# Kernel optimization log

Measured on AMD Instinct MI355X. Metric: run time of the kernel, lower is better.

The kernel has to match this reference:

```python
import jax, jax.numpy as jnp
import numpy as np

N_NODES = 10000
N_EDGES = 640000
IN_CH = 128
HID = 128
OUT = 2


def setup_inputs() -> dict:
    key = jax.random.key(0)
    ks = jax.random.split(key, 12)
    s_in = 1.0 / np.sqrt(IN_CH)
    s_2h = 1.0 / np.sqrt(2 * HID)
    s_h = 1.0 / np.sqrt(HID)
    return {
        "x": jax.random.normal(ks[0], (N_NODES, IN_CH), dtype=jnp.float32),
        "edge_index": jax.random.randint(ks[1], (2, N_EDGES), 0, N_NODES, dtype=jnp.int64),
        # SAGEConv: lin_l applied to aggregated neighbors (has bias), lin_r to self (no bias)
        "W_l": jax.random.uniform(ks[2], (IN_CH, HID), jnp.float32, -s_in, s_in),
        "b_l": jax.random.uniform(ks[3], (HID,), jnp.float32, -s_in, s_in),
        "W_r": jax.random.uniform(ks[4], (IN_CH, HID), jnp.float32, -s_in, s_in),
        # lin0: in -> hid
        "W0": jax.random.uniform(ks[5], (IN_CH, HID), jnp.float32, -s_in, s_in),
        "b0": jax.random.uniform(ks[6], (HID,), jnp.float32, -s_in, s_in),
        # lin1: 2*hid -> hid
        "W1": jax.random.uniform(ks[7], (2 * HID, HID), jnp.float32, -s_2h, s_2h),
        "b1": jax.random.uniform(ks[8], (HID,), jnp.float32, -s_2h, s_2h),
        # lin2: hid -> out
        "W2": jax.random.uniform(ks[9], (HID, OUT), jnp.float32, -s_h, s_h),
        "b2": jax.random.uniform(ks[10], (OUT,), jnp.float32, -s_h, s_h),
    }


def reference(x, edge_index, W_l, b_l, W_r, W0, b0, W1, b1, W2, b2):
    src, dst = edge_index[0], edge_index[1]
    # SAGE mean aggregation: gather source features, scatter-mean onto dst nodes
    msgs = x[src]                                                # [E, in]
    agg = jax.ops.segment_sum(msgs, dst, num_segments=N_NODES)  # [N, in]
    deg = jax.ops.segment_sum(jnp.ones((src.shape[0],), x.dtype), dst,
                              num_segments=N_NODES)              # [N]
    agg = agg / jnp.maximum(deg, 1.0)[:, None]
    # SAGEConv output: lin_l(agg) + lin_r(x)
    h = agg @ W_l + b_l + x @ W_r                                # [N, hid]
    h = jax.nn.relu(h)
    h = jnp.max(h, axis=-2)                                      # [hid] global max pool over nodes
    # concat branch: news node is x[0]
    news = jax.nn.relu(x[0] @ W0 + b0)                           # [hid]
    h = jax.nn.relu(jnp.concatenate([news, h], axis=-1) @ W1 + b1)
    return h @ W2 + b2                                           # [out]
```

## Files before the change

### kernel.cpp

```cpp
#include <hip/hip_runtime.h>
#include <hip/hip_bf16.h>

#define NCH 128
#define NPART 256
#define NRANGE 512
#define SEGCAP 24
#define RCAP 2560
#define PSMAX 32

typedef __attribute__((ext_vector_type(8))) short bfrag;
typedef __attribute__((ext_vector_type(4))) float ffrag;
typedef __attribute__((ext_vector_type(2))) float f32x2;

__device__ inline unsigned int f2bf_pair(float lo, float hi) {
    unsigned int ul = __float_as_uint(lo);
    unsigned int uh = __float_as_uint(hi);
    ul = (ul + 0x7fffu + ((ul >> 16) & 1u)) >> 16;
    uh = (uh + 0x7fffu + ((uh >> 16) & 1u)) & 0xffff0000u;
    return (ul & 0xffffu) | uh;
}

__global__ __launch_bounds__(256) void k_partprep(
    const float2* __restrict__ x2, const float* __restrict__ Wl,
    const float* __restrict__ Wr, const int* __restrict__ ei32,
    const long long* __restrict__ ei64, unsigned int* __restrict__ M32,
    unsigned int* __restrict__ Wt32, unsigned short* __restrict__ xq,
    unsigned int* __restrict__ seg, int* __restrict__ segcnt,
    unsigned int* __restrict__ hmaxU, int* __restrict__ done,
    int n2, int N, int E, int PSr) {
    const int t = threadIdx.x;
    if (blockIdx.x < NPART) {
        if (blockIdx.x == 0) {
            if (t < 128) hmaxU[t] = 0u;
            if (t == 128) *done = 0;
        }
        __shared__ int sflag;
        __shared__ int cur[NRANGE];
        if (t < 64) {
            int v = ei32[2 * t + 1];
            unsigned long long b = __ballot(v != 0);
            if (t == 0) sflag = (b == 0ULL) ? 1 : 0;
        }
        for (int i = t; i < NRANGE; i += 256) cur[i] = 0;
        __syncthreads();
        const int flag = sflag;
        const int b = blockIdx.x;
        const int ES = (E + NPART - 1) / NPART;
        const int e0 = b * ES, e1 = min(E, e0 + ES);
        for (int bb = e0; bb < e1; bb += 1024) {
            int ebase = bb + t * 4;
            int m = min(4, e1 - ebase);
            if (m <= 0) continue;
            int src4[4], dst4[4];
            if (flag) {
#pragma unroll
                for (int j = 0; j < 4; ++j) {
                    if (j < m) {
                        src4[j] = (int)ei64[ebase + j];
                        dst4[j] = (int)ei64[(size_t)E + ebase + j];
                    }
                }
            } else {
#pragma unroll
                for (int j = 0; j < 4; ++j) {
                    if (j < m) {
                        src4[j] = ei32[ebase + j];
                        dst4[j] = ei32[(size_t)E + ebase + j];
                    }
                }
            }
#pragma unroll
            for (int j = 0; j < 4; ++j) {
                if (j < m) {
                    int r = dst4[j] / PSr;
                    int dl = dst4[j] - r * PSr;
                    int pos = atomicAdd(&cur[r], 1);
                    if (pos < SEGCAP)
                        seg[((size_t)b * NRANGE + r) * SEGCAP + pos] =
                            ((unsigned int)dl << 16) | (unsigned int)src4[j];
                }
            }
        }
        __syncthreads();
        for (int i = t; i < NRANGE; i += 256)
            segcnt[b * NRANGE + i] = min(cur[i], SEGCAP);
        return;
    }
    int i = (int)(blockIdx.x - NPART) * 256 + t;
    if (i < n2) {
        float2 v = x2[i];
        int n = i >> 6, c = i & 63;
        M32[n * 128 + 64 + c] = f2bf_pair(v.x, v.y);
        xq[i] = (unsigned short)__builtin_amdgcn_cvt_pk_fp8_f32(v.x, v.y, 0u, false);
        return;
    }
    int j = i - n2;
    if (j < 128 * 128) {
        int c = j & 127, kp = j >> 7;
        int k0 = 2 * kp, k1 = 2 * kp + 1;
        float v0 = (k0 < 128) ? Wl[k0 * 128 + c] : Wr[(k0 - 128) * 128 + c];
        float v1 = (k1 < 128) ? Wl[k1 * 128 + c] : Wr[(k1 - 128) * 128 + c];
        Wt32[c * 128 + kp] = f2bf_pair(v0, v1);
    }
}

__global__ __launch_bounds__(512) void k_aggdense(
    const unsigned int* __restrict__ seg, const int* __restrict__ segcnt,
    const unsigned int* __restrict__ M32, const unsigned short* __restrict__ xq,
    const short* __restrict__ Wt, const float* __restrict__ bl,
    unsigned int* __restrict__ hmaxU, int* __restrict__ done,
    const float* __restrict__ x,
    const float* __restrict__ W0, const float* __restrict__ b0,
    const float* __restrict__ W1, const float* __restrict__ b1,
    const float* __restrict__ W2, const float* __restrict__ b2,
    float* __restrict__ out, int N, int PSr) {
    __shared__ unsigned int tmp[RCAP];
    __shared__ unsigned short scsr[RCAP];
    __shared__ unsigned int aggL[PSMAX * 66];
    __shared__ int sc[NPART];
    __shared__ int hist[PSMAX], startp[PSMAX], cur[PSMAX];
    __shared__ float red[8][32];
    __shared__ int lastflag;
    const int r = blockIdx.x;
    const int t = threadIdx.x;

    int mycnt = 0;
    if (t < NPART) { mycnt = segcnt[t * NRANGE + r]; sc[t] = mycnt; }
    for (int i = t; i < PSMAX * 66; i += 512) aggL[i] = 0;
    if (t < PSMAX) hist[t] = 0;
    __syncthreads();
    for (int off = 1; off < NPART; off <<= 1) {
        int v = (t >= off && t < NPART) ? sc[t - off] : 0;
        __syncthreads();
        if (t < NPART) sc[t] += v;
        __syncthreads();
    }
    const int total = min(sc[NPART - 1], RCAP);

    if (t < NPART && mycnt > 0) {
        int excl = sc[t] - mycnt;
        const uint4* sp = (const uint4*)(seg + ((size_t)t * NRANGE + r) * SEGCAP);
        for (int k = 0; k < mycnt; k += 4) {
            uint4 v = sp[k >> 2];
            unsigned int w[4] = {v.x, v.y, v.z, v.w};
#pragma unroll
            for (int j = 0; j < 4; ++j) {
                if (k + j < mycnt) {
                    unsigned int e = w[j];
                    tmp[excl + k + j] = e;
                    atomicAdd(&hist[e >> 16], 1);
                }
            }
        }
    }
    __syncthreads();
    if (t == 0) {
        int run = 0;
#pragma unroll
        for (int i = 0; i < PSMAX; ++i) { startp[i] = run; cur[i] = run; run += hist[i]; }
    }
    __syncthreads();
    for (int i = t; i < total; i += 512) {
        unsigned int v = tmp[i];
        int pos = atomicAdd(&cur[v >> 16], 1);
        scsr[pos] = (unsigned short)(v & 0xffffu);
    }
    __syncthreads();

    const int wave = t >> 6, lane = t & 63;
    for (int li = wave; li < PSr; li += 8) {
        int node = r * PSr + li;
        if (node >= N) break;
        int base = startp[li], d = hist[li];
        float ax = 0.f, ay = 0.f;
        int i = 0;
        for (; i + 16 <= d; i += 16) {
            int s[16];
            unsigned short u[16];
#pragma unroll
            for (int j = 0; j < 16; ++j) s[j] = scsr[base + i + j];
#pragma unroll
            for (int j = 0; j < 16; ++j) u[j] = xq[s[j] * 64 + lane];
#pragma unroll
            for (int j = 0; j < 16; ++j) {
                f32x2 v = __builtin_amdgcn_cvt_pk_f32_fp8((unsigned int)u[j], false);
                ax += v.x; ay += v.y;
            }
        }
        for (; i + 8 <= d; i += 8) {
            int s[8];
            unsigned short u[8];
#pragma unroll
            for (int j = 0; j < 8; ++j) s[j] = scsr[base + i + j];
#pragma unroll
            for (int j = 0; j < 8; ++j) u[j] = xq[s[j] * 64 + lane];
#pragma unroll
            for (int j = 0; j < 8; ++j) {
                f32x2 v = __builtin_amdgcn_cvt_pk_f32_fp8((unsigned int)u[j], false);
                ax += v.x; ay += v.y;
            }
        }
        for (; i < d; ++i) {
            unsigned short u = xq[((int)scsr[base + i]) * 64 + lane];
            f32x2 v = __builtin_amdgcn_cvt_pk_f32_fp8((unsigned int)u, false);
            ax += v.x; ay += v.y;
        }
        float sca = 1.0f / fmaxf((float)d, 1.0f);
        aggL[li * 66 + lane] = f2bf_pair(ax * sca, ay * sca);
    }
    __syncthreads();

    const int l16 = lane & 15, quad = lane >> 4;
    const int rt = wave & 1, cg = wave >> 1;
    const int lrow = rt * 16 + l16;
    bfrag a[8];
#pragma unroll
    for (int kk = 0; kk < 4; ++kk)
        a[kk] = *(const bfrag*)((const short*)(aggL + lrow * 66 + kk * 16 + quad * 4));
    {
        int mc = min(r * PSr + lrow, N - 1);
#pragma unroll
        for (int kk = 0; kk < 4; ++kk)
            a[4 + kk] = *(const bfrag*)((const short*)(M32 + (size_t)mc * 128 + 64)
                                        + kk * 32 + quad * 8);
    }
    float mx[2];
#pragma unroll
    for (int ct = 0; ct < 2; ++ct) {
        int col = cg * 32 + ct * 16 + l16;
        float bv = bl[col];
        ffrag acc = {bv, bv, bv, bv};
        const short* wp = Wt + (size_t)col * 256 + quad * 8;
#pragma unroll
        for (int kk = 0; kk < 8; ++kk) {
            bfrag b = *(const bfrag*)(wp + kk * 32);
            acc = __builtin_amdgcn_mfma_f32_16x16x32_bf16(a[kk], b, acc, 0, 0, 0);
        }
        float lm = 0.f;
#pragma unroll
        for (int rr = 0; rr < 4; ++rr) {
            int lr = rt * 16 + quad * 4 + rr;
            int nd = r * PSr + lr;
            if (lr < PSr && nd < N) lm = fmaxf(lm, fmaxf(acc[rr], 0.f));
        }
        lm = fmaxf(lm, __shfl_xor(lm, 16));
        lm = fmaxf(lm, __shfl_xor(lm, 32));
        mx[ct] = lm;
    }
    if (lane < 16) {
        red[wave][l16]      = mx[0];
        red[wave][16 + l16] = mx[1];
    }
    __syncthreads();
    if (t < 128) {
        int cg2 = t >> 5, wi = t & 31;
        float v = fmaxf(red[2 * cg2][wi], red[2 * cg2 + 1][wi]);
        atomicMax(&hmaxU[t], __float_as_uint(v));
    }

    __syncthreads();
    if (t == 0) {
        __threadfence();
        int old = atomicAdd(done, 1);
        lastflag = (old == NRANGE - 1) ? 1 : 0;
    }
    __syncthreads();
    if (!lastflag) return;
    __threadfence();

    float* hs   = (float*)tmp;
    float* cat  = hs;
    float* part = hs + 256;
    float* h1p  = hs + 768;
    float* pr   = hs + 896;
    float* xsp  = hs + 1152;
    const int c = t & 127, sg = t >> 7;
    if (t < 128) {
        xsp[t] = x[t];
        cat[128 + t] = __uint_as_float(atomicOr(&hmaxU[t], 0u));
    }
    __syncthreads();
    {
        float a0 = 0.f, a1 = 0.f, a2 = 0.f, a3 = 0.f;
        int k0 = sg * 32;
#pragma unroll
        for (int j = 0; j < 32; j += 4) {
            a0 += xsp[k0 + j + 0] * W0[(k0 + j + 0) * NCH + c];
            a1 += xsp[k0 + j + 1] * W0[(k0 + j + 1) * NCH + c];
            a2 += xsp[k0 + j + 2] * W0[(k0 + j + 2) * NCH + c];
            a3 += xsp[k0 + j + 3] * W0[(k0 + j + 3) * NCH + c];
        }
        part[sg * 128 + c] = (a0 + a1) + (a2 + a3);
    }
    __syncthreads();
    if (t < 128)
        cat[t] = fmaxf(b0[t] + part[t] + part[128 + t] + part[256 + t] + part[384 + t], 0.f);
    __syncthreads();
    {
        float a0 = 0.f, a1 = 0.f, a2 = 0.f, a3 = 0.f;
        int k0 = sg * 64;
#pragma unroll
        for (int j = 0; j < 64; j += 4) {
            a0 += cat[k0 + j + 0] * W1[(k0 + j + 0) * NCH + c];
            a1 += cat[k0 + j + 1] * W1[(k0 + j + 1) * NCH + c];
            a2 += cat[k0 + j + 2] * W1[(k0 + j + 2) * NCH + c];
            a3 += cat[k0 + j + 3] * W1[(k0 + j + 3) * NCH + c];
        }
        part[sg * 128 + c] = (a0 + a1) + (a2 + a3);
    }
    __syncthreads();
    if (t < 128)
        h1p[t] = fmaxf(b1[t] + part[t] + part[128 + t] + part[256 + t] + part[384 + t], 0.f);
    __syncthreads();
    if (t < 128) {
        float2 w = ((const float2*)W2)[t];
        pr[t]       = h1p[t] * w.x;
        pr[128 + t] = h1p[t] * w.y;
    }
    __syncthreads();
    for (int off = 64; off >= 1; off >>= 1) {
        if (t < off) { pr[t] += pr[t + off]; pr[128 + t] += pr[128 + t + off]; }
        __syncthreads();
    }
    if (t == 0) out[0] = pr[0] + b2[0];
    if (t == 1) out[1] = pr[128] + b2[1];
}

__global__ void k_detect(const int* __restrict__ ei, int* __restrict__ flag) {
    int v = ei[2 * threadIdx.x + 1];
    unsigned long long b = __ballot(v != 0);
    if (threadIdx.x == 0) *flag = (b == 0ULL) ? 1 : 0;
}
__global__ void k_hist(const int* __restrict__ ei32, const long long* __restrict__ ei64,
                       const int* __restrict__ flag, int* __restrict__ cnt, int E) {
    int e = blockIdx.x * blockDim.x + threadIdx.x;
    if (e >= E) return;
    int dst = (*flag) ? (int)ei64[(size_t)E + e] : ei32[(size_t)E + e];
    atomicAdd(&cnt[dst], 1);
}
__global__ void k_scan(const int* __restrict__ cnt, int* __restrict__ row_start, int N) {
    __shared__ int lds[1024];
    int t = threadIdx.x;
    int chunk = (N + 1023) / 1024;
    int base = t * chunk;
    int sum = 0;
    for (int i = 0; i < chunk; ++i) {
        int idx = base + i;
        if (idx < N) sum += cnt[idx];
    }
    lds[t] = sum;
    __syncthreads();
    for (int off = 1; off < 1024; off <<= 1) {
        int v = (t >= off) ? lds[t - off] : 0;
        __syncthreads();
        lds[t] += v;
        __syncthreads();
    }
    int run = (t == 0) ? 0 : lds[t - 1];
    for (int i = 0; i < chunk; ++i) {
        int idx = base + i;
        if (idx < N) { row_start[idx] = run; run += cnt[idx]; }
    }
    if (t == 1023) row_start[N] = run;
}
__global__ void k_fill(const int* __restrict__ ei32, const long long* __restrict__ ei64,
                       const int* __restrict__ flag, const int* __restrict__ row_start,
                       int* __restrict__ cursor, int* __restrict__ csr, int E) {
    int e = blockIdx.x * blockDim.x + threadIdx.x;
    if (e >= E) return;
    int src, dst;
    if (*flag) { src = (int)ei64[e]; dst = (int)ei64[(size_t)E + e]; }
    else       { src = ei32[e];      dst = ei32[(size_t)E + e]; }
    int pos = atomicAdd(&cursor[dst], 1);
    csr[row_start[dst] + pos] = src;
}
__global__ __launch_bounds__(256) void k_agg_linmax(
    const float* __restrict__ x, const int* __restrict__ row_start,
    const int* __restrict__ csr, const float* __restrict__ Wl,
    const float* __restrict__ bl, const float* __restrict__ Wr,
    unsigned int* __restrict__ hmaxU, int N, int E) {
    const int lane = threadIdx.x & 63;
    const int wave = threadIdx.x >> 6;
    const int group = blockIdx.x * 4 + wave;
    const int ngroups = (N + 3) / 4;
    const float2* __restrict__ x2  = (const float2*)x;
    const float2* __restrict__ Wl2 = (const float2*)Wl;
    const float2* __restrict__ Wr2 = (const float2*)Wr;
    const float2* __restrict__ bl2 = (const float2*)bl;
    float2 m = make_float2(0.f, 0.f);
    if (group < ngroups) {
        int n0 = group * 4;
        int s[4], d[4];
#pragma unroll
        for (int q = 0; q < 4; ++q) {
            int n = n0 + q;
            if (n < N) { s[q] = row_start[n]; d[q] = row_start[n + 1] - s[q]; }
            else       { s[q] = 0; d[q] = 0; }
        }
        int maxd = max(max(d[0], d[1]), max(d[2], d[3]));
        float2 acc[4];
#pragma unroll
        for (int q = 0; q < 4; ++q) acc[q] = make_float2(0.f, 0.f);
        int idxv[4] = {0, 0, 0, 0};
        for (int i = 0; i < maxd; ++i) {
            int t = i & 63;
            if (t == 0) {
#pragma unroll
                for (int q = 0; q < 4; ++q) {
                    if (i < d[q]) {
                        int a = s[q] + i + lane;
                        a = (a < E) ? a : (E - 1);
                        idxv[q] = csr[a];
                    }
                }
            }
#pragma unroll
            for (int q = 0; q < 4; ++q) {
                if (i < d[q]) {
                    int src = __shfl(idxv[q], t);
                    float2 v = x2[src * 64 + lane];
                    acc[q].x += v.x; acc[q].y += v.y;
                }
            }
        }
        float2 xv[4];
#pragma unroll
        for (int q = 0; q < 4; ++q) {
            float sc = 1.0f / fmaxf((float)d[q], 1.0f);
            acc[q].x *= sc; acc[q].y *= sc;
            int n = n0 + q;
            xv[q] = (n < N) ? x2[n * 64 + lane] : make_float2(0.f, 0.f);
        }
        float2 o[4];
#pragma unroll
        for (int q = 0; q < 4; ++q) o[q] = bl2[lane];
        for (int j = 0; j < 64; ++j) {
            float2 wl0 = Wl2[(2 * j) * 64 + lane];
            float2 wl1 = Wl2[(2 * j + 1) * 64 + lane];
            float2 wr0 = Wr2[(2 * j) * 64 + lane];
            float2 wr1 = Wr2[(2 * j + 1) * 64 + lane];
#pragma unroll
            for (int q = 0; q < 4; ++q) {
                float ax = __shfl(acc[q].x, j);
                float ay = __shfl(acc[q].y, j);
                float xx = __shfl(xv[q].x, j);
                float xy = __shfl(xv[q].y, j);
                o[q].x += ax * wl0.x + ay * wl1.x + xx * wr0.x + xy * wr1.x;
                o[q].y += ax * wl0.y + ay * wl1.y + xx * wr0.y + xy * wr1.y;
            }
        }
#pragma unroll
        for (int q = 0; q < 4; ++q) {
            if (n0 + q < N) {
                m.x = fmaxf(m.x, fmaxf(o[q].x, 0.f));
                m.y = fmaxf(m.y, fmaxf(o[q].y, 0.f));
            }
        }
    }
    __shared__ float2 red2[4][64];
    red2[wave][lane] = m;
    __syncthreads();
    if (wave == 0) {
#pragma unroll
        for (int ww = 1; ww < 4; ++ww) {
            m.x = fmaxf(m.x, red2[ww][lane].x);
            m.y = fmaxf(m.y, red2[ww][lane].y);
        }
        atomicMax(&hmaxU[2 * lane],     __float_as_uint(m.x));
        atomicMax(&hmaxU[2 * lane + 1], __float_as_uint(m.y));
    }
}
__global__ void k_head_fb(const float* __restrict__ x, const float* __restrict__ hmax,
                          const float* __restrict__ W0, const float* __restrict__ b0,
                          const float* __restrict__ W1, const float* __restrict__ b1,
                          const float* __restrict__ W2, const float* __restrict__ b2,
                          float* __restrict__ out) {
    __shared__ float s_cat[2 * NCH];
    __shared__ float s_part[256];
    __shared__ float s_h1[NCH];
    int t = threadIdx.x;
    if (t < NCH) {
        float acc = b0[t];
        for (int k = 0; k < NCH; ++k) acc += x[k] * W0[k * NCH + t];
        s_cat[t] = fmaxf(acc, 0.f);
        s_cat[NCH + t] = hmax[t];
    }
    __syncthreads();
    {
        int c = t & 127, half = t >> 7;
        float p = 0.f;
        int k0 = half * NCH;
        for (int k = k0; k < k0 + NCH; ++k) p += s_cat[k] * W1[k * NCH + c];
        s_part[t] = p;
    }
    __syncthreads();
    if (t < NCH) s_h1[t] = fmaxf(s_part[t] + s_part[NCH + t] + b1[t], 0.f);
    __syncthreads();
    if (t < 2) {
        float o = b2[t];
        for (int k = 0; k < NCH; ++k) o += s_h1[k] * W2[k * 2 + t];
        out[t] = o;
    }
}

extern "C" void kernel_launch(void* const* d_in, const int* in_sizes, int n_in,
                              void* d_out, int out_size, void* d_ws, size_t ws_size,
                              hipStream_t stream) {
    const float* x  = (const float*)d_in[0];
    const void*  ei = d_in[1];
    const float* Wl = (const float*)d_in[2];
    const float* bl = (const float*)d_in[3];
    const float* Wr = (const float*)d_in[4];
    const float* W0 = (const float*)d_in[5];
    const float* b0 = (const float*)d_in[6];
    const float* W1 = (const float*)d_in[7];
    const float* b1 = (const float*)d_in[8];
    const float* W2 = (const float*)d_in[9];
    const float* b2 = (const float*)d_in[10];
    float* out = (float*)d_out;

    const int N = in_sizes[0] / NCH;
    const int E = in_sizes[1] / 2;
    const int n2 = N * 64;
    const int PSr = (N + NRANGE - 1) / NRANGE;

    int* iws = (int*)d_ws;
    unsigned int* hmaxU = (unsigned int*)iws;
    int* done = iws + 128;
    int* segcnt = iws + 192;
    unsigned int* seg = (unsigned int*)(segcnt + NPART * NRANGE);
    unsigned int* Wt32 = seg + (size_t)NPART * NRANGE * SEGCAP;
    unsigned int* M32  = Wt32 + 128 * 128;
    unsigned short* xq = (unsigned short*)(M32 + (size_t)N * 128);
    size_t need = ((size_t)192 + NPART * NRANGE +
                   (size_t)NPART * NRANGE * SEGCAP + 128 * 128 +
                   (size_t)N * 128 + (size_t)N * 32) * 4;
    bool main_ok = (need <= ws_size) && (N <= NRANGE * PSMAX) && (N <= 65535) &&
                   (PSr >= 1) && (PSr <= PSMAX);

    if (main_ok) {
        int prepb = (n2 + 128 * 128 + 255) / 256;
        k_partprep<<<NPART + prepb, 256, 0, stream>>>(
            (const float2*)x, Wl, Wr, (const int*)ei, (const long long*)ei,
            M32, Wt32, xq, seg, segcnt, hmaxU, done, n2, N, E, PSr);
        k_aggdense<<<NRANGE, 512, 0, stream>>>(seg, segcnt, M32, xq,
                                               (const short*)Wt32,
                                               bl, hmaxU, done, x,
                                               W0, b0, W1, b1, W2, b2, out, N, PSr);
        return;
    }

    int* fcnt      = iws;
    int* fcursor   = iws + N;
    unsigned int* fhmax = (unsigned int*)(iws + 2 * N);
    int* flag      = iws + 2 * N + 128;
    int* frs       = iws + 2 * N + 132;
    int* fcsr      = iws + 3 * N + 144;

    hipMemsetAsync(d_ws, 0, (size_t)(2 * N + 128) * sizeof(int), stream);
    k_detect<<<1, 64, 0, stream>>>((const int*)ei, flag);
    k_hist<<<(E + 255) / 256, 256, 0, stream>>>((const int*)ei, (const long long*)ei,
                                                flag, fcnt, E);
    k_scan<<<1, 1024, 0, stream>>>(fcnt, frs, N);
    k_fill<<<(E + 255) / 256, 256, 0, stream>>>((const int*)ei, (const long long*)ei,
                                                flag, frs, fcursor, fcsr, E);
    int ngroups = (N + 3) / 4;
    k_agg_linmax<<<(ngroups + 3) / 4, 256, 0, stream>>>(x, frs, fcsr, Wl, bl, Wr,
                                                        fhmax, N, E);
    k_head_fb<<<1, 256, 0, stream>>>(x, (const float*)fhmax, W0, b0, W1, b1, W2, b2, out);
}
```

Before: 122.8 us.

## Widen fp8 gather to 4 channels per lane, use wave-shuffle scans and magic division

The neighbor gather now has each half-wave load 32-bit words holding four fp8 channels and process alternate edges, then combines the halves with a cross-half shuffle. This aims for fewer, wider gather loads and more memory parallelism per wave. The block-wide prefix sums over partitions and histogram bins become wave shuffle scans to cut barriers, and the per-edge division by PSr becomes a precomputed multiply-high. The prep kernel also vectorizes the x conversion to float4. The tail path now gathers with clamped indices, which may do redundant loads.

```diff
diff --git a/kernel.cpp b/kernel.cpp
--- a/kernel.cpp
+++ b/kernel.cpp
@@ -21,13 +21,13 @@
 }
 
 __global__ __launch_bounds__(256) void k_partprep(
-    const float2* __restrict__ x2, const float* __restrict__ Wl,
+    const float4* __restrict__ x4, const float* __restrict__ Wl,
     const float* __restrict__ Wr, const int* __restrict__ ei32,
     const long long* __restrict__ ei64, unsigned int* __restrict__ M32,
-    unsigned int* __restrict__ Wt32, unsigned short* __restrict__ xq,
+    unsigned int* __restrict__ Wt32, unsigned int* __restrict__ xqU,
     unsigned int* __restrict__ seg, int* __restrict__ segcnt,
     unsigned int* __restrict__ hmaxU, int* __restrict__ done,
-    int n2, int N, int E, int PSr) {
+    int nq, int N, int E, int PSr, unsigned int Mdiv) {
     const int t = threadIdx.x;
     if (blockIdx.x < NPART) {
         if (blockIdx.x == 0) {
@@ -72,8 +72,9 @@
 #pragma unroll
             for (int j = 0; j < 4; ++j) {
                 if (j < m) {
-                    int r = dst4[j] / PSr;
-                    int dl = dst4[j] - r * PSr;
+                    int dstj = dst4[j];
+                    int r = Mdiv ? (int)__umulhi((unsigned int)dstj, Mdiv) : dstj;
+                    int dl = dstj - r * PSr;
                     int pos = atomicAdd(&cur[r], 1);
                     if (pos < SEGCAP)
                         seg[((size_t)b * NRANGE + r) * SEGCAP + pos] =
@@ -87,14 +88,18 @@
         return;
     }
     int i = (int)(blockIdx.x - NPART) * 256 + t;
-    if (i < n2) {
-        float2 v = x2[i];
-        int n = i >> 6, c = i & 63;
-        M32[n * 128 + 64 + c] = f2bf_pair(v.x, v.y);
-        xq[i] = (unsigned short)__builtin_amdgcn_cvt_pk_fp8_f32(v.x, v.y, 0u, false);
+    if (i < nq) {
+        float4 v = x4[i];
+        int n = i >> 5, cq = i & 31;
+        unsigned int p0 = f2bf_pair(v.x, v.y);
+        unsigned int p1 = f2bf_pair(v.z, v.w);
+        *(uint2*)(M32 + (size_t)n * 128 + 64 + 2 * cq) = make_uint2(p0, p1);
+        unsigned int q = __builtin_amdgcn_cvt_pk_fp8_f32(v.x, v.y, 0u, false);
+        q = __builtin_amdgcn_cvt_pk_fp8_f32(v.z, v.w, q, true);
+        xqU[(size_t)n * 32 + cq] = q;
         return;
     }
-    int j = i - n2;
+    int j = i - nq;
     if (j < 128 * 128) {
         int c = j & 127, kp = j >> 7;
         int k0 = 2 * kp, k1 = 2 * kp + 1;
@@ -117,28 +122,34 @@
     __shared__ unsigned int tmp[RCAP];
     __shared__ unsigned short scsr[RCAP];
     __shared__ unsigned int aggL[PSMAX * 66];
-    __shared__ int sc[NPART];
+    __shared__ int wtot[4];
     __shared__ int hist[PSMAX], startp[PSMAX], cur[PSMAX];
     __shared__ float red[8][32];
     __shared__ int lastflag;
     const int r = blockIdx.x;
     const int t = threadIdx.x;
+    const int wave = t >> 6, lane = t & 63;
 
     int mycnt = 0;
-    if (t < NPART) { mycnt = segcnt[t * NRANGE + r]; sc[t] = mycnt; }
+    if (t < NPART) mycnt = segcnt[t * NRANGE + r];
     for (int i = t; i < PSMAX * 66; i += 512) aggL[i] = 0;
     if (t < PSMAX) hist[t] = 0;
-    __syncthreads();
-    for (int off = 1; off < NPART; off <<= 1) {
-        int v = (t >= off && t < NPART) ? sc[t - off] : 0;
-        __syncthreads();
-        if (t < NPART) sc[t] += v;
-        __syncthreads();
-    }
-    const int total = min(sc[NPART - 1], RCAP);
+    int incl = mycnt;
+    if (wave < 4) {
+#pragma unroll
+        for (int off = 1; off < 64; off <<= 1) {
+            int u = __shfl_up(incl, off);
+            if (lane >= off) incl += u;
+        }
+        if (lane == 63) wtot[wave] = incl;
+    }
+    __syncthreads();
+    const int tt0 = wtot[0], tt1 = wtot[1], tt2 = wtot[2], tt3 = wtot[3];
+    const int total = min(tt0 + tt1 + tt2 + tt3, RCAP);
 
     if (t < NPART && mycnt > 0) {
-        int excl = sc[t] - mycnt;
+        int wadd = (wave > 0 ? tt0 : 0) + (wave > 1 ? tt1 : 0) + (wave > 2 ? tt2 : 0);
+        int excl = incl + wadd - mycnt;
         const uint4* sp = (const uint4*)(seg + ((size_t)t * NRANGE + r) * SEGCAP);
         for (int k = 0; k < mycnt; k += 4) {
             uint4 v = sp[k >> 2];
@@ -154,10 +165,16 @@
         }
     }
     __syncthreads();
-    if (t == 0) {
-        int run = 0;
-#pragma unroll
-        for (int i = 0; i < PSMAX; ++i) { startp[i] = run; cur[i] = run; run += hist[i]; }
+    if (t < 32) {
+        int h = hist[t];
+        int ip = h;
+#pragma unroll
+        for (int off = 1; off < 32; off <<= 1) {
+            int u = __shfl_up(ip, off);
+            if (lane >= off) ip += u;
+        }
+        startp[t] = ip - h;
+        cur[t] = ip - h;
     }
     __syncthreads();
     for (int i = t; i < total; i += 512) {
@@ -167,46 +184,57 @@
     }
     __syncthreads();
 
-    const int wave = t >> 6, lane = t & 63;
+    const unsigned int* __restrict__ xqU = (const unsigned int*)xq;
+    const int half = lane >> 5, lq = lane & 31;
     for (int li = wave; li < PSr; li += 8) {
         int node = r * PSr + li;
         if (node >= N) break;
         int base = startp[li], d = hist[li];
-        float ax = 0.f, ay = 0.f;
+        float a0 = 0.f, a1 = 0.f, a2 = 0.f, a3 = 0.f;
         int i = 0;
-        for (; i + 16 <= d; i += 16) {
+        for (; i + 32 <= d; i += 32) {
             int s[16];
-            unsigned short u[16];
-#pragma unroll
-            for (int j = 0; j < 16; ++j) s[j] = scsr[base + i + j];
-#pragma unroll
-            for (int j = 0; j < 16; ++j) u[j] = xq[s[j] * 64 + lane];
+            unsigned int u[16];
+#pragma unroll
+            for (int j = 0; j < 16; ++j) s[j] = scsr[base + i + 2 * j + half];
+#pragma unroll
+            for (int j = 0; j < 16; ++j) u[j] = xqU[s[j] * 32 + lq];
 #pragma unroll
             for (int j = 0; j < 16; ++j) {
-                f32x2 v = __builtin_amdgcn_cvt_pk_f32_fp8((unsigned int)u[j], false);
-                ax += v.x; ay += v.y;
-            }
-        }
-        for (; i + 8 <= d; i += 8) {
-            int s[8];
-            unsigned short u[8];
-#pragma unroll
-            for (int j = 0; j < 8; ++j) s[j] = scsr[base + i + j];
-#pragma unroll
-            for (int j = 0; j < 8; ++j) u[j] = xq[s[j] * 64 + lane];
-#pragma unroll
-            for (int j = 0; j < 8; ++j) {
-                f32x2 v = __builtin_amdgcn_cvt_pk_f32_fp8((unsigned int)u[j], false);
-                ax += v.x; ay += v.y;
-            }
-        }
-        for (; i < d; ++i) {
-            unsigned short u = xq[((int)scsr[base + i]) * 64 + lane];
-            f32x2 v = __builtin_amdgcn_cvt_pk_f32_fp8((unsigned int)u, false);
-            ax += v.x; ay += v.y;
-        }
+                f32x2 v0 = __builtin_amdgcn_cvt_pk_f32_fp8(u[j], false);
+                f32x2 v1 = __builtin_amdgcn_cvt_pk_f32_fp8(u[j], true);
+                a0 += v0.x; a1 += v0.y; a2 += v1.x; a3 += v1.y;
+            }
+        }
+        if (i < d) {
+            int s[16];
+            unsigned int u[16];
+#pragma unroll
+            for (int j = 0; j < 16; ++j) {
+                int idx = i + 2 * j + half;
+                s[j] = scsr[base + min(idx, d - 1)];
+            }
+#pragma unroll
+            for (int j = 0; j < 16; ++j) u[j] = xqU[s[j] * 32 + lq];
+#pragma unroll
+            for (int j = 0; j < 16; ++j) {
+                int idx = i + 2 * j + half;
+                if (idx < d) {
+                    f32x2 v0 = __builtin_amdgcn_cvt_pk_f32_fp8(u[j], false);
+                    f32x2 v1 = __builtin_amdgcn_cvt_pk_f32_fp8(u[j], true);
+                    a0 += v0.x; a1 += v0.y; a2 += v1.x; a3 += v1.y;
+                }
+            }
+        }
+        a0 += __shfl_xor(a0, 32);
+        a1 += __shfl_xor(a1, 32);
+        a2 += __shfl_xor(a2, 32);
+        a3 += __shfl_xor(a3, 32);
         float sca = 1.0f / fmaxf((float)d, 1.0f);
-        aggL[li * 66 + lane] = f2bf_pair(ax * sca, ay * sca);
+        if (half == 0) {
+            aggL[li * 66 + 2 * lq]     = f2bf_pair(a0 * sca, a1 * sca);
+            aggL[li * 66 + 2 * lq + 1] = f2bf_pair(a2 * sca, a3 * sca);
+        }
     }
     __syncthreads();
 
@@ -521,7 +549,7 @@
 
     const int N = in_sizes[0] / NCH;
     const int E = in_sizes[1] / 2;
-    const int n2 = N * 64;
+    const int nq = N * 32;
     const int PSr = (N + NRANGE - 1) / NRANGE;
 
     int* iws = (int*)d_ws;
@@ -539,10 +567,14 @@
                    (PSr >= 1) && (PSr <= PSMAX);
 
     if (main_ok) {
-        int prepb = (n2 + 128 * 128 + 255) / 256;
+        unsigned int Mdiv = (PSr > 1)
+            ? (unsigned int)(0x100000000ULL / (unsigned long long)PSr + 1ULL)
+            : 0u;
+        int prepb = (nq + 128 * 128 + 255) / 256;
         k_partprep<<<NPART + prepb, 256, 0, stream>>>(
-            (const float2*)x, Wl, Wr, (const int*)ei, (const long long*)ei,
-            M32, Wt32, xq, seg, segcnt, hmaxU, done, n2, N, E, PSr);
+            (const float4*)x, Wl, Wr, (const int*)ei, (const long long*)ei,
+            M32, Wt32, (unsigned int*)xq, seg, segcnt, hmaxU, done, nq, N, E,
+            PSr, Mdiv);
         k_aggdense<<<NRANGE, 512, 0, stream>>>(seg, segcnt, M32, xq,
                                                (const short*)Wt32,
                                                bl, hmaxU, done, x,
```

Result: faster. 118.9 us (-3.2%).
